# Optimization experiments

Measured on AMD Instinct MI355X. Metric: run time of the kernel, lower is better.

Reference implementation:

```python
import jax, jax.numpy as jnp
import numpy as np

W_WIN = 5        # fine_window_size
D_F = 128        # fine d_model
D_C = 256        # coarse d_model
B, HF, WF = 2, 208, 208
WC = 104
LC = WC * WC
N = 5000


def setup_inputs() -> dict:
    key = jax.random.key(0)
    ks = jax.random.split(key, 12)
    inp = {
        'feat_f0': jax.random.normal(ks[0], (B, D_F, HF, WF), jnp.float32),
        'feat_f1': jax.random.normal(ks[1], (B, D_F, HF, WF), jnp.float32),
        'feat_c0': jax.random.normal(ks[2], (B, LC, D_C), jnp.float32),
        'feat_c1': jax.random.normal(ks[3], (B, LC, D_C), jnp.float32),
        # linear layer params (stored as [in, out]; torch weight is [out, in])
        'corr_fuse_w': jax.random.normal(ks[4], (3 * D_F, D_F), jnp.float32) * 0.05,
        'corr_fuse_b': jnp.zeros((D_F,), jnp.float32),
        'down_proj_w': jax.random.normal(ks[5], (D_C, D_F), jnp.float32) * 0.05,
        'down_proj_b': jnp.zeros((D_F,), jnp.float32),
        'merge_feat_w': jax.random.normal(ks[6], (2 * D_F, D_F), jnp.float32) * 0.05,
        'merge_feat_b': jnp.zeros((D_F,), jnp.float32),
        'b_ids': jax.random.randint(ks[7], (N,), 0, B),
        'i_ids': jax.random.randint(ks[8], (N,), 0, LC),
        'j_ids': jax.random.randint(ks[9], (N,), 0, LC),
        'w0c': WC,
        'w1c': WC,
    }
    return inp


def _extract_patches(feat, b_ids, x_ids, y_ids, W):
    # Equivalent to F.unfold(feat, W, stride=1, padding=W//2) followed by a
    # gather at linear index y*width+x: directly gather the WxW window
    # centered at (x, y) with zero padding. feat: [B, C, H, Wd].
    Bsz, C, H, Wd = feat.shape
    off = jnp.arange(W) - W // 2
    yy = (y_ids[:, None] + off)[:, :, None]          # [n, W, 1]
    xx = (x_ids[:, None] + off)[:, None, :]          # [n, 1, W]
    valid = (yy >= 0) & (yy < H) & (xx >= 0) & (xx < Wd)  # [n, W, W]
    yc = jnp.clip(yy, 0, H - 1)
    xc = jnp.clip(xx, 0, Wd - 1)
    # advanced-index gather -> [n, W, W, C] (kernel rows outer, cols inner,
    # channel last: matches unfold's C-major layout after view/transpose)
    p = feat[b_ids[:, None, None], :, yc, xc]
    p = p * valid[..., None].astype(feat.dtype)
    return p.reshape(p.shape[0], W * W, C)           # [n, ww, C]


def reference(feat_f0, feat_f1, feat_c0, feat_c1,
              corr_fuse_w, corr_fuse_b, down_proj_w, down_proj_b,
              merge_feat_w, merge_feat_b,
              b_ids, i_ids, j_ids, w0c, w1c):
    W = W_WIN
    ww = W * W
    d_f = feat_f0.shape[1]
    Hf0, Wf0 = feat_f0.shape[2], feat_f0.shape[3]
    Hf1, Wf1 = feat_f1.shape[2], feat_f1.shape[3]

    x0 = jnp.clip((i_ids % w0c) * 2, 0, Wf0 - 1)
    y0 = jnp.clip((i_ids // w0c) * 2, 0, Hf0 - 1)
    x1 = jnp.clip((j_ids % w1c) * 2, 0, Wf1 - 1)
    y1 = jnp.clip((j_ids // w1c) * 2, 0, Hf1 - 1)

    p0 = _extract_patches(feat_f0, b_ids, x0, y0, W)   # [N, ww, d_f]
    p1 = _extract_patches(feat_f1, b_ids, x1, y1, W)

    inv_s = 1.0 / (d_f ** 0.5)
    c_patch = p0 * p1 * inv_s
    ctx_map = feat_f1.mean(axis=(2, 3))[b_ids][:, None, :]   # [N, 1, d_f]
    c_uav = p0 * ctx_map * inv_s
    ctx_uav = feat_f0.mean(axis=(2, 3))[b_ids][:, None, :]
    c_map = p1 * ctx_uav * inv_s

    f0 = jnp.concatenate([c_patch, c_uav, c_map], -1) @ corr_fuse_w + corr_fuse_b
    f1 = jnp.concatenate([c_patch, c_map, c_uav], -1) @ corr_fuse_w + corr_fuse_b

    # cat_c_feat branch
    fc = jnp.concatenate([feat_c0[b_ids, i_ids], feat_c1[b_ids, j_ids]], 0)
    fc = fc @ down_proj_w + down_proj_b                       # [2N, d_f]
    fc_rep = jnp.broadcast_to(fc[:, None, :], (fc.shape[0], ww, fc.shape[1]))
    merged = jnp.concatenate([jnp.concatenate([f0, f1], 0), fc_rep], -1)
    merged = merged @ merge_feat_w + merge_feat_b             # [2N, ww, d_f]

    n = f0.shape[0]
    return merged[:n], merged[n:]
```

## Files before the change

kernel.cpp:

```cpp
#include <hip/hip_runtime.h>

#define HF   208
#define WF   208
#define D_C  256
#define LC   10816
#define NPTS 5000
#define HW   (HF*WF)
#define INV_S 0.08838834764831845f
#define PAD  136

#define G_BLOCKS    625
#define PREP_BLOCKS 641
#define TR_BLOCKS   2704
#define PTG_GRID    (G_BLOCKS + PREP_BLOCKS + TR_BLOCKS)

typedef __bf16 bf16_t;
typedef __bf16 bf16x8 __attribute__((ext_vector_type(8)));
typedef float  f32x4  __attribute__((ext_vector_type(4)));

#define FTR_OFF   172032
#define FTR_BYTES ((size_t)2*2*HW*128*2)
#define G_OFF     (FTR_OFF + FTR_BYTES)
#define G_BYTES   ((size_t)2*NPTS*128*4)

__global__ __launch_bounds__(256, 8) void ptg_kernel(
    const float* __restrict__ f0, const float* __restrict__ f1,
    const float* __restrict__ fc0, const float* __restrict__ fc1,
    const float* __restrict__ corr_w, const float* __restrict__ corr_b,
    const float* __restrict__ dp_w,   const float* __restrict__ dp_b,
    const float* __restrict__ mg_w,   const float* __restrict__ mg_b,
    const int* __restrict__ b_ids, const int* __restrict__ i_ids,
    const int* __restrict__ j_ids,
    bf16_t* __restrict__ A_swz, bf16_t* __restrict__ DmB,
    float* __restrict__ bias_all,
    bf16_t* __restrict__ ftr, float* __restrict__ ctxs,
    float* __restrict__ g) {
  __shared__ __align__(16) union {
    struct { bf16_t tile[64][136]; float cred[128]; } tr;
    float s_src[16][256];
  } sm;
  int bid = blockIdx.x;
  int tid = threadIdx.x;

  int prep_id = -1;
  if (gridDim.x == 641) {
    prep_id = bid;
  } else if (bid >= G_BLOCKS && bid < G_BLOCKS + PREP_BLOCKS) {
    prep_id = bid - G_BLOCKS;
  }

  if (prep_id >= 0) {
    if (tid >= 128) return;
    int c = tid;
    if (prep_id < 384) {
      int mat = prep_id >> 7, r = prep_id & 127;
      float acc = 0.f;
      for (int t = 0; t < 128; ++t)
        acc += corr_w[(mat * 128 + r) * 128 + t] * mg_w[t * 128 + c];
      if (mat == 0) acc *= INV_S;
      int ks = r >> 5, quad = (r & 31) >> 3, jj = r & 7;
      int nt = c >> 4, lr = c & 15;
      A_swz[mat * 16384 + (((nt * 4 + ks) * 64) + quad * 16 + lr) * 8 + jj] = (bf16_t)acc;
    } else if (prep_id < 640) {
      int r = prep_id - 384;
      float acc = 0.f;
      for (int t = 0; t < 128; ++t)
        acc += dp_w[r * 128 + t] * mg_w[(128 + t) * 128 + c];
      DmB[(((r >> 3) * 128) + c) * 8 + (r & 7)] = (bf16_t)acc;
    } else {
      float acc = mg_b[c];
      for (int t = 0; t < 128; ++t) {
        acc += corr_b[t] * mg_w[t * 128 + c];
        acc += dp_b[t]   * mg_w[(128 + t) * 128 + c];
      }
      bias_all[c] = acc;
    }
    return;
  }

  if (bid < G_BLOCKS) {
    int r0 = bid * 16;
    for (int u = tid; u < 16 * 256; u += 256) {
      int rr = u >> 8, t = u & 255;
      int r = r0 + rr;
      const float* src;
      int b, idx;
      if (r < NPTS) { b = b_ids[r]; idx = i_ids[r]; src = fc0; }
      else          { b = b_ids[r - NPTS]; idx = j_ids[r - NPTS]; src = fc1; }
      sm.s_src[rr][t] = src[((size_t)b * LC + idx) * D_C + t];
    }
    __syncthreads();
    int col = tid & 127, half = tid >> 7;
    float h[8];
    {
      float db = dp_b[col];
#pragma unroll
      for (int r8 = 0; r8 < 8; ++r8) h[r8] = db;
      for (int t = 0; t < 256; t += 4) {
        f32x4 wv;
#pragma unroll
        for (int k = 0; k < 4; ++k) wv[k] = dp_w[(t + k) * 128 + col];
#pragma unroll
        for (int r8 = 0; r8 < 8; ++r8) {
          f32x4 sv = *(const f32x4*)&sm.s_src[half * 8 + r8][t];
          h[r8] += sv[0] * wv[0] + sv[1] * wv[1] + sv[2] * wv[2] + sv[3] * wv[3];
        }
      }
    }
    __syncthreads();
    float* s_h = &sm.s_src[0][0];
#pragma unroll
    for (int r8 = 0; r8 < 8; ++r8) s_h[(half * 8 + r8) * 128 + col] = h[r8];
    __syncthreads();
    float acc2[8];
    float mb = mg_b[col];
#pragma unroll
    for (int r8 = 0; r8 < 8; ++r8) acc2[r8] = mb;
    for (int t = 0; t < 128; t += 4) {
      f32x4 wv;
#pragma unroll
      for (int k = 0; k < 4; ++k) wv[k] = mg_w[(128 + t + k) * 128 + col];
#pragma unroll
      for (int r8 = 0; r8 < 8; ++r8) {
        f32x4 sv = *(const f32x4*)&s_h[(half * 8 + r8) * 128 + t];
        acc2[r8] += sv[0] * wv[0] + sv[1] * wv[1] + sv[2] * wv[2] + sv[3] * wv[3];
      }
    }
    float cp = 0.f;
    for (int t = 0; t < 128; ++t) cp += corr_b[t] * mg_w[t * 128 + col];
#pragma unroll
    for (int r8 = 0; r8 < 8; ++r8)
      g[(size_t)(r0 + half * 8 + r8) * 128 + col] = acc2[r8] + cp;
    return;
  }

  int tbid = bid - (G_BLOCKS + PREP_BLOCKS);
  int tb = tbid / 676;
  int hw0 = (tbid % 676) * 64;
  const float* src = (tb < 2 ? f0 : f1) + (size_t)((tb & 1) * 128) * HW;
  int wg = tid & 15, cr = tid >> 4;
  int w4 = wg * 4;
  float csum[8];
#pragma unroll
  for (int k = 0; k < 8; ++k) {
    int c = cr + k * 16;
    f32x4 v = *(const f32x4*)&src[(size_t)c * HW + hw0 + w4];
    csum[k] = (v[0] + v[1]) + (v[2] + v[3]);
#pragma unroll
    for (int j = 0; j < 4; ++j) sm.tr.tile[w4 + j][c] = (bf16_t)v[j];
  }
#pragma unroll
  for (int k = 0; k < 8; ++k) {
    float s = csum[k];
    s += __shfl_down(s, 8, 16);
    s += __shfl_down(s, 4, 16);
    s += __shfl_down(s, 2, 16);
    s += __shfl_down(s, 1, 16);
    if (wg == 0) sm.tr.cred[cr + k * 16] = s;
  }
  __syncthreads();
  if (tid < 128) atomicAdd(&ctxs[tb * 128 + tid], sm.tr.cred[tid]);
  bf16_t* dst = ftr + ((size_t)tb * HW + hw0) * 128;
  int cb = wg * 8;
#pragma unroll
  for (int i = 0; i < 4; ++i) {
    int p = cr + 16 * i;
    bf16x8 v = *(const bf16x8*)&sm.tr.tile[p][cb];
    *(bf16x8*)(dst + (size_t)p * 128 + cb) = v;
  }
}

__global__ __launch_bounds__(256, 6) void main_kernel(
    const bf16_t* __restrict__ ftr,
    const int* __restrict__ b_ids, const int* __restrict__ i_ids,
    const int* __restrict__ j_ids, const int* __restrict__ w0c_p,
    const int* __restrict__ w1c_p, const float* __restrict__ ctxs,
    const bf16_t* __restrict__ A_swz, const float* __restrict__ g,
    float* __restrict__ out) {
  __shared__ __align__(16) union {
    bf16_t sV[3][32][PAD];
    float  so[2][25 * 128];
  } sm;

  int n = blockIdx.x;
  int tid = threadIdx.x;
  int b = b_ids[n], ii = i_ids[n], jj = j_ids[n];
  int w0c = w0c_p[0], w1c = w1c_p[0];
  int x0 = min((ii % w0c) * 2, WF - 1), y0 = min((ii / w0c) * 2, HF - 1);
  int x1 = min((jj % w1c) * 2, WF - 1), y1 = min((jj / w1c) * 2, HF - 1);

  int grp = tid >> 3, e = tid & 7;
  if (grp < 25) {
    const bf16_t* base0 = ftr + (size_t)b * HW * 128;
    const bf16_t* base1 = ftr + (size_t)(2 + b) * HW * 128;
    int dy = grp / 5 - 2, dx = grp % 5 - 2;
    int ya = y0 + dy, xa = x0 + dx;
    int yb = y1 + dy, xb = x1 + dx;
    bool v0 = (ya >= 0 && ya < HF && xa >= 0 && xa < WF);
    bool v1 = (yb >= 0 && yb < HF && xb >= 0 && xb < WF);
    const bf16_t* r0 = base0 + ((size_t)(v0 ? ya * WF + xa : 0)) * 128;
    const bf16_t* r1 = base1 + ((size_t)(v1 ? yb * WF + xb : 0)) * 128;
    const float ksc = INV_S / (float)HW;
#pragma unroll
    for (int h = 0; h < 2; ++h) {
      int cb = h * 64 + e * 8;
      bf16x8 a0 = *(const bf16x8*)(r0 + cb);
      bf16x8 a1 = *(const bf16x8*)(r1 + cb);
      f32x4 cs0a = *(const f32x4*)&ctxs[b * 128 + cb];
      f32x4 cs0b = *(const f32x4*)&ctxs[b * 128 + cb + 4];
      f32x4 cs1a = *(const f32x4*)&ctxs[256 + b * 128 + cb];
      f32x4 cs1b = *(const f32x4*)&ctxs[256 + b * 128 + cb + 4];
      bf16x8 oP, o1, o2;
#pragma unroll
      for (int j = 0; j < 8; ++j) {
        float p0 = v0 ? (float)a0[j] : 0.f;
        float p1 = v1 ? (float)a1[j] : 0.f;
        float c0f = (j < 4 ? cs0a[j & 3] : cs0b[j & 3]) * ksc;
        float c1f = (j < 4 ? cs1a[j & 3] : cs1b[j & 3]) * ksc;
        oP[j] = (bf16_t)(p0 * p1);
        o1[j] = (bf16_t)(p0 * c1f);
        o2[j] = (bf16_t)(p1 * c0f);
      }
      *(bf16x8*)&sm.sV[0][grp][cb] = oP;
      *(bf16x8*)&sm.sV[1][grp][cb] = o1;
      *(bf16x8*)&sm.sV[2][grp][cb] = o2;
    }
  }
  __syncthreads();

  int w = tid >> 6, lane = tid & 63, quad = lane >> 4, lr = lane & 15;
  f32x4 accP[2][2] = {};
  f32x4 acc01[2][2] = {};
  f32x4 acc10[2][2] = {};

#pragma unroll
  for (int ks = 0; ks < 4; ++ks) {
    bf16x8 va[2][3];
#pragma unroll
    for (int mt = 0; mt < 2; ++mt)
#pragma unroll
      for (int m = 0; m < 3; ++m)
        va[mt][m] = *(const bf16x8*)&sm.sV[m][mt * 16 + lr][ks * 32 + quad * 8];
    bf16x8 vb[3][2];
#pragma unroll
    for (int m = 0; m < 3; ++m)
#pragma unroll
      for (int ntl = 0; ntl < 2; ++ntl) {
        int nt = w * 2 + ntl;
        vb[m][ntl] = *(const bf16x8*)(A_swz + m * 16384 + (((nt * 4 + ks) * 64) + lane) * 8);
      }
#pragma unroll
    for (int mt = 0; mt < 2; ++mt)
#pragma unroll
      for (int ntl = 0; ntl < 2; ++ntl) {
        accP[mt][ntl]  = __builtin_amdgcn_mfma_f32_16x16x32_bf16(va[mt][0], vb[0][ntl], accP[mt][ntl], 0, 0, 0);
        acc01[mt][ntl] = __builtin_amdgcn_mfma_f32_16x16x32_bf16(va[mt][1], vb[1][ntl], acc01[mt][ntl], 0, 0, 0);
        acc01[mt][ntl] = __builtin_amdgcn_mfma_f32_16x16x32_bf16(va[mt][2], vb[2][ntl], acc01[mt][ntl], 0, 0, 0);
        acc10[mt][ntl] = __builtin_amdgcn_mfma_f32_16x16x32_bf16(va[mt][2], vb[1][ntl], acc10[mt][ntl], 0, 0, 0);
        acc10[mt][ntl] = __builtin_amdgcn_mfma_f32_16x16x32_bf16(va[mt][1], vb[2][ntl], acc10[mt][ntl], 0, 0, 0);
      }
  }
  __syncthreads();

#pragma unroll
  for (int ntl = 0; ntl < 2; ++ntl) {
    int col = w * 32 + ntl * 16 + lr;
#pragma unroll
    for (int mt = 0; mt < 2; ++mt)
#pragma unroll
      for (int rg = 0; rg < 4; ++rg) {
        int row = mt * 16 + quad * 4 + rg;
        if (row < 25) {
          sm.so[0][row * 128 + col] = accP[mt][ntl][rg] + acc01[mt][ntl][rg];
          sm.so[1][row * 128 + col] = accP[mt][ntl][rg] + acc10[mt][ntl][rg];
        }
      }
  }
  __syncthreads();

  float* o0 = out + (size_t)n * 3200;
  float* o1 = out + (size_t)NPTS * 3200 + (size_t)n * 3200;
  const float* g0 = g + (size_t)n * 128;
  const float* g1 = g + (size_t)(NPTS + n) * 128;
  for (int i = tid; i < 800; i += 256) {
    int f = i * 4, c = f & 127;
    f32x4 gv0 = *(const f32x4*)(g0 + c);
    f32x4 gv1 = *(const f32x4*)(g1 + c);
    f32x4 v0 = *(const f32x4*)&sm.so[0][f];
    f32x4 v1 = *(const f32x4*)&sm.so[1][f];
    __builtin_nontemporal_store(v0 + gv0, (f32x4*)(o0 + f));
    __builtin_nontemporal_store(v1 + gv1, (f32x4*)(o1 + f));
  }
}

__global__ __launch_bounds__(256) void ctx_mean_f32_kernel(
    const float* __restrict__ f0, const float* __restrict__ f1,
    float* __restrict__ ctxs) {
  int id = blockIdx.x;
  const float* src = (id < 256 ? f0 : f1) + (size_t)(id & 255) * HW;
  float s = 0.f;
  for (int i = threadIdx.x; i < HW; i += 256) s += src[i];
  for (int off = 32; off > 0; off >>= 1) s += __shfl_down(s, off, 64);
  __shared__ float part[4];
  if ((threadIdx.x & 63) == 0) part[threadIdx.x >> 6] = s;
  __syncthreads();
  if (threadIdx.x == 0) ctxs[id] = part[0] + part[1] + part[2] + part[3];
}

__global__ __launch_bounds__(256, 4) void main_fallback_kernel(
    const float* __restrict__ f0, const float* __restrict__ f1,
    const float* __restrict__ fc0, const float* __restrict__ fc1,
    const int* __restrict__ b_ids, const int* __restrict__ i_ids,
    const int* __restrict__ j_ids, const int* __restrict__ w0c_p,
    const int* __restrict__ w1c_p, const float* __restrict__ ctxs,
    const float* __restrict__ bias_all, const bf16_t* __restrict__ A_swz,
    const bf16_t* __restrict__ DmB, float* __restrict__ out) {
  __shared__ __align__(16) bf16_t sV[3][32][PAD];
  __shared__ float sg[2][128];
  int n = blockIdx.x;
  int tid = threadIdx.x;
  int b = b_ids[n], ii = i_ids[n], jj = j_ids[n];
  int w0c = w0c_p[0], w1c = w1c_p[0];
  int x0 = min((ii % w0c) * 2, WF - 1), y0 = min((ii / w0c) * 2, HF - 1);
  int x1 = min((jj % w1c) * 2, WF - 1), y1 = min((jj / w1c) * 2, HF - 1);
  const float ksc = INV_S / (float)HW;
  int c = tid & 127, kh = tid >> 7;
  float cs0 = ctxs[b * 128 + c] * ksc;
  float cs1 = ctxs[256 + b * 128 + c] * ksc;
  const float* f0b = f0 + (size_t)(b * 128 + c) * HW;
  const float* f1b = f1 + (size_t)(b * 128 + c) * HW;
  for (int k = kh; k < 32; k += 2) {
    float p0 = 0.f, p1 = 0.f;
    if (k < 25) {
      int dy = k / 5 - 2, dx = k % 5 - 2;
      int ya = y0 + dy, xa = x0 + dx;
      if (ya >= 0 && ya < HF && xa >= 0 && xa < WF) p0 = f0b[ya * WF + xa];
      int yb = y1 + dy, xb = x1 + dx;
      if (yb >= 0 && yb < HF && xb >= 0 && xb < WF) p1 = f1b[yb * WF + xb];
    }
    sV[0][k][c] = (bf16_t)(p0 * p1);
    sV[1][k][c] = (bf16_t)(p0 * cs1);
    sV[2][k][c] = (bf16_t)(p1 * cs0);
  }
  {
    int h = tid >> 7, col = tid & 127;
    const float* fcrow = h ? fc1 + ((size_t)b * LC + jj) * D_C
                           : fc0 + ((size_t)b * LC + ii) * D_C;
    const bf16_t* dbase = DmB + col * 8;
    float p0 = 0.f, p1 = 0.f, p2 = 0.f, p3 = 0.f;
#pragma unroll 4
    for (int t8 = 0; t8 < 32; ++t8) {
      bf16x8 d  = *(const bf16x8*)(dbase + t8 * 1024);
      f32x4  fa = *(const f32x4*)(fcrow + t8 * 8);
      f32x4  fb = *(const f32x4*)(fcrow + t8 * 8 + 4);
      p0 += fa[0] * (float)d[0] + fb[0] * (float)d[4];
      p1 += fa[1] * (float)d[1] + fb[1] * (float)d[5];
      p2 += fa[2] * (float)d[2] + fb[2] * (float)d[6];
      p3 += fa[3] * (float)d[3] + fb[3] * (float)d[7];
    }
    sg[h][col] = ((p0 + p1) + (p2 + p3));
  }
  __syncthreads();
  int w = tid >> 6, lane = tid & 63, quad = lane >> 4, lr = lane & 15;
  f32x4 accP[2][2] = {}, acc01[2][2] = {}, acc10[2][2] = {};
#pragma unroll
  for (int ks = 0; ks < 4; ++ks) {
    bf16x8 va[2][3];
#pragma unroll
    for (int mt = 0; mt < 2; ++mt)
#pragma unroll
      for (int m = 0; m < 3; ++m)
        va[mt][m] = *(const bf16x8*)&sV[m][mt * 16 + lr][ks * 32 + quad * 8];
    bf16x8 vb[3][2];
#pragma unroll
    for (int m = 0; m < 3; ++m)
#pragma unroll
      for (int ntl = 0; ntl < 2; ++ntl) {
        int nt = w * 2 + ntl;
        vb[m][ntl] = *(const bf16x8*)(A_swz + m * 16384 + (((nt * 4 + ks) * 64) + lane) * 8);
      }
#pragma unroll
    for (int mt = 0; mt < 2; ++mt)
#pragma unroll
      for (int ntl = 0; ntl < 2; ++ntl) {
        accP[mt][ntl]  = __builtin_amdgcn_mfma_f32_16x16x32_bf16(va[mt][0], vb[0][ntl], accP[mt][ntl], 0, 0, 0);
        acc01[mt][ntl] = __builtin_amdgcn_mfma_f32_16x16x32_bf16(va[mt][1], vb[1][ntl], acc01[mt][ntl], 0, 0, 0);
        acc01[mt][ntl] = __builtin_amdgcn_mfma_f32_16x16x32_bf16(va[mt][2], vb[2][ntl], acc01[mt][ntl], 0, 0, 0);
        acc10[mt][ntl] = __builtin_amdgcn_mfma_f32_16x16x32_bf16(va[mt][2], vb[1][ntl], acc10[mt][ntl], 0, 0, 0);
        acc10[mt][ntl] = __builtin_amdgcn_mfma_f32_16x16x32_bf16(va[mt][1], vb[2][ntl], acc10[mt][ntl], 0, 0, 0);
      }
  }
#pragma unroll
  for (int ntl = 0; ntl < 2; ++ntl) {
    int col = w * 32 + ntl * 16 + lr;
    float bg = bias_all[col];
    float gg0 = sg[0][col] + bg, gg1 = sg[1][col] + bg;
#pragma unroll
    for (int mt = 0; mt < 2; ++mt)
#pragma unroll
      for (int rg = 0; rg < 4; ++rg) {
        int row = mt * 16 + quad * 4 + rg;
        if (row < 25) {
          size_t o = ((size_t)n * 25 + row) * 128 + col;
          out[o] = accP[mt][ntl][rg] + acc01[mt][ntl][rg] + gg0;
          out[(size_t)NPTS * 25 * 128 + o] = accP[mt][ntl][rg] + acc10[mt][ntl][rg] + gg1;
        }
      }
  }
}

extern "C" void kernel_launch(void* const* d_in, const int* in_sizes, int n_in,
                              void* d_out, int out_size, void* d_ws, size_t ws_size,
                              hipStream_t stream) {
  const float* f0     = (const float*)d_in[0];
  const float* f1     = (const float*)d_in[1];
  const float* fc0    = (const float*)d_in[2];
  const float* fc1    = (const float*)d_in[3];
  const float* corr_w = (const float*)d_in[4];
  const float* corr_b = (const float*)d_in[5];
  const float* dp_w   = (const float*)d_in[6];
  const float* dp_b   = (const float*)d_in[7];
  const float* mg_w   = (const float*)d_in[8];
  const float* mg_b   = (const float*)d_in[9];
  const int* b_ids    = (const int*)d_in[10];
  const int* i_ids    = (const int*)d_in[11];
  const int* j_ids    = (const int*)d_in[12];
  const int* w0c      = (const int*)d_in[13];
  const int* w1c      = (const int*)d_in[14];

  char* ws = (char*)d_ws;
  float*  ctxs     = (float*)(ws);
  float*  bias_all = (float*)(ws + 4096);
  bf16_t* A_swz    = (bf16_t*)(ws + 8192);
  bf16_t* DmB      = (bf16_t*)(ws + 106496);
  bf16_t* ftr      = (bf16_t*)(ws + FTR_OFF);
  float*  g        = (float*)(ws + G_OFF);
  int fast = (ws_size >= G_OFF + G_BYTES) ? 1 : 0;

  if (fast) {
    hipMemsetAsync(ctxs, 0, 2048, stream);
    ptg_kernel<<<PTG_GRID, 256, 0, stream>>>(
        f0, f1, fc0, fc1, corr_w, corr_b, dp_w, dp_b, mg_w, mg_b,
        b_ids, i_ids, j_ids, A_swz, DmB, bias_all, ftr, ctxs, g);
    main_kernel<<<NPTS, 256, 0, stream>>>(ftr, b_ids, i_ids, j_ids, w0c, w1c,
                                          ctxs, A_swz, g, (float*)d_out);
  } else {
    ptg_kernel<<<641, 256, 0, stream>>>(
        f0, f1, fc0, fc1, corr_w, corr_b, dp_w, dp_b, mg_w, mg_b,
        b_ids, i_ids, j_ids, A_swz, DmB, bias_all, ftr, ctxs, g);
    ctx_mean_f32_kernel<<<512, 256, 0, stream>>>(f0, f1, ctxs);
    main_fallback_kernel<<<NPTS, 256, 0, stream>>>(f0, f1, fc0, fc1, b_ids,
                                                   i_ids, j_ids, w0c, w1c, ctxs,
                                                   bias_all, A_swz, DmB,
                                                   (float*)d_out);
  }
}
```

Measured before the change: 330.0 us.

## Vectorize coarse-feature GEMV blocks and swizzle transpose tile to avoid bank conflicts

The G blocks in the prep kernel now use f32x4 loads for the gathered coarse rows and weights. Each thread computes 4 output columns for 2 rows, and the redundant per-thread corr_b·mg_w dot product is dropped. That bias term now comes from bias_all, which main_kernel adds in its epilogue. The transpose blocks load all 8 vectors first, then write into LDS with an XOR swizzle on the channel index, cutting LDS bank conflicts during the bf16 transpose. This adds one extra bias load per output vector in main_kernel.

Result: faster. 322.6 us (-2.3%).

```diff
diff --git a/kernel.cpp b/kernel.cpp
--- a/kernel.cpp
+++ b/kernel.cpp
@@ -80,57 +80,52 @@
 
   if (bid < G_BLOCKS) {
     int r0 = bid * 16;
-    for (int u = tid; u < 16 * 256; u += 256) {
-      int rr = u >> 8, t = u & 255;
-      int r = r0 + rr;
-      const float* src;
-      int b, idx;
-      if (r < NPTS) { b = b_ids[r]; idx = i_ids[r]; src = fc0; }
-      else          { b = b_ids[r - NPTS]; idx = j_ids[r - NPTS]; src = fc1; }
-      sm.s_src[rr][t] = src[((size_t)b * LC + idx) * D_C + t];
+    {
+      int l = tid & 63, wv = tid >> 6;
+      for (int k2 = 0; k2 < 4; ++k2) {
+        int rr = wv * 4 + k2;
+        int r = r0 + rr;
+        const float* src;
+        int b, idx;
+        if (r < NPTS) { b = b_ids[r]; idx = i_ids[r]; src = fc0; }
+        else          { b = b_ids[r - NPTS]; idx = j_ids[r - NPTS]; src = fc1; }
+        f32x4 val = *(const f32x4*)&src[((size_t)b * LC + idx) * D_C + l * 4];
+        *(f32x4*)&sm.s_src[rr][l * 4] = val;
+      }
     }
     __syncthreads();
-    int col = tid & 127, half = tid >> 7;
-    float h[8];
-    {
-      float db = dp_b[col];
-#pragma unroll
-      for (int r8 = 0; r8 < 8; ++r8) h[r8] = db;
-      for (int t = 0; t < 256; t += 4) {
-        f32x4 wv;
-#pragma unroll
-        for (int k = 0; k < 4; ++k) wv[k] = dp_w[(t + k) * 128 + col];
-#pragma unroll
-        for (int r8 = 0; r8 < 8; ++r8) {
-          f32x4 sv = *(const f32x4*)&sm.s_src[half * 8 + r8][t];
-          h[r8] += sv[0] * wv[0] + sv[1] * wv[1] + sv[2] * wv[2] + sv[3] * wv[3];
-        }
-      }
+    int cg = tid & 31, rg = tid >> 5;
+    const f32x4* dpw4 = (const f32x4*)dp_w;
+    f32x4 h0 = {0.f, 0.f, 0.f, 0.f}, h1 = {0.f, 0.f, 0.f, 0.f};
+    for (int t = 0; t < 256; t += 4) {
+      f32x4 w0 = dpw4[(t + 0) * 32 + cg];
+      f32x4 w1 = dpw4[(t + 1) * 32 + cg];
+      f32x4 w2 = dpw4[(t + 2) * 32 + cg];
+      f32x4 w3 = dpw4[(t + 3) * 32 + cg];
+      f32x4 s0 = *(const f32x4*)&sm.s_src[rg * 2][t];
+      f32x4 s1 = *(const f32x4*)&sm.s_src[rg * 2 + 1][t];
+      h0 += w0 * s0[0] + w1 * s0[1] + w2 * s0[2] + w3 * s0[3];
+      h1 += w0 * s1[0] + w1 * s1[1] + w2 * s1[2] + w3 * s1[3];
     }
     __syncthreads();
     float* s_h = &sm.s_src[0][0];
-#pragma unroll
-    for (int r8 = 0; r8 < 8; ++r8) s_h[(half * 8 + r8) * 128 + col] = h[r8];
+    *(f32x4*)&s_h[(rg * 2) * 128 + cg * 4]     = h0;
+    *(f32x4*)&s_h[(rg * 2 + 1) * 128 + cg * 4] = h1;
     __syncthreads();
-    float acc2[8];
-    float mb = mg_b[col];
-#pragma unroll
-    for (int r8 = 0; r8 < 8; ++r8) acc2[r8] = mb;
+    const f32x4* mgw4 = (const f32x4*)(mg_w + 128 * 128);
+    f32x4 a0 = {0.f, 0.f, 0.f, 0.f}, a1 = {0.f, 0.f, 0.f, 0.f};
     for (int t = 0; t < 128; t += 4) {
-      f32x4 wv;
-#pragma unroll
-      for (int k = 0; k < 4; ++k) wv[k] = mg_w[(128 + t + k) * 128 + col];
-#pragma unroll
-      for (int r8 = 0; r8 < 8; ++r8) {
-        f32x4 sv = *(const f32x4*)&s_h[(half * 8 + r8) * 128 + t];
-        acc2[r8] += sv[0] * wv[0] + sv[1] * wv[1] + sv[2] * wv[2] + sv[3] * wv[3];
-      }
-    }
-    float cp = 0.f;
-    for (int t = 0; t < 128; ++t) cp += corr_b[t] * mg_w[t * 128 + col];
-#pragma unroll
-    for (int r8 = 0; r8 < 8; ++r8)
-      g[(size_t)(r0 + half * 8 + r8) * 128 + col] = acc2[r8] + cp;
+      f32x4 w0 = mgw4[(t + 0) * 32 + cg];
+      f32x4 w1 = mgw4[(t + 1) * 32 + cg];
+      f32x4 w2 = mgw4[(t + 2) * 32 + cg];
+      f32x4 w3 = mgw4[(t + 3) * 32 + cg];
+      f32x4 s0 = *(const f32x4*)&s_h[(rg * 2) * 128 + t];
+      f32x4 s1 = *(const f32x4*)&s_h[(rg * 2 + 1) * 128 + t];
+      a0 += w0 * s0[0] + w1 * s0[1] + w2 * s0[2] + w3 * s0[3];
+      a1 += w0 * s1[0] + w1 * s1[1] + w2 * s1[2] + w3 * s1[3];
+    }
+    *(f32x4*)&g[(size_t)(r0 + rg * 2) * 128 + cg * 4]     = a0;
+    *(f32x4*)&g[(size_t)(r0 + rg * 2 + 1) * 128 + cg * 4] = a1;
     return;
   }
 
@@ -140,14 +135,21 @@
   const float* src = (tb < 2 ? f0 : f1) + (size_t)((tb & 1) * 128) * HW;
   int wg = tid & 15, cr = tid >> 4;
   int w4 = wg * 4;
-  float csum[8];
+  f32x4 v[8];
 #pragma unroll
   for (int k = 0; k < 8; ++k) {
     int c = cr + k * 16;
-    f32x4 v = *(const f32x4*)&src[(size_t)c * HW + hw0 + w4];
-    csum[k] = (v[0] + v[1]) + (v[2] + v[3]);
-#pragma unroll
-    for (int j = 0; j < 4; ++j) sm.tr.tile[w4 + j][c] = (bf16_t)v[j];
+    v[k] = *(const f32x4*)&src[(size_t)c * HW + hw0 + w4];
+  }
+  float csum[8];
+  int wmask = wg & 7;
+#pragma unroll
+  for (int k = 0; k < 8; ++k) {
+    int c = cr + k * 16;
+    csum[k] = (v[k][0] + v[k][1]) + (v[k][2] + v[k][3]);
+    int cs = (((c >> 3) ^ wmask) << 3) | (c & 7);
+#pragma unroll
+    for (int j = 0; j < 4; ++j) sm.tr.tile[w4 + j][cs] = (bf16_t)v[k][j];
   }
 #pragma unroll
   for (int k = 0; k < 8; ++k) {
@@ -161,12 +163,12 @@
   __syncthreads();
   if (tid < 128) atomicAdd(&ctxs[tb * 128 + tid], sm.tr.cred[tid]);
   bf16_t* dst = ftr + ((size_t)tb * HW + hw0) * 128;
-  int cb = wg * 8;
 #pragma unroll
   for (int i = 0; i < 4; ++i) {
     int p = cr + 16 * i;
-    bf16x8 v = *(const bf16x8*)&sm.tr.tile[p][cb];
-    *(bf16x8*)(dst + (size_t)p * 128 + cb) = v;
+    int cs = (wg ^ ((p >> 2) & 7)) << 3;
+    bf16x8 vv = *(const bf16x8*)&sm.tr.tile[p][cs];
+    *(bf16x8*)(dst + (size_t)p * 128 + wg * 8) = vv;
   }
 }
 
@@ -176,7 +178,7 @@
     const int* __restrict__ j_ids, const int* __restrict__ w0c_p,
     const int* __restrict__ w1c_p, const float* __restrict__ ctxs,
     const bf16_t* __restrict__ A_swz, const float* __restrict__ g,
-    float* __restrict__ out) {
+    const float* __restrict__ bias_all, float* __restrict__ out) {
   __shared__ __align__(16) union {
     bf16_t sV[3][32][PAD];
     float  so[2][25 * 128];
@@ -284,8 +286,9 @@
   const float* g1 = g + (size_t)(NPTS + n) * 128;
   for (int i = tid; i < 800; i += 256) {
     int f = i * 4, c = f & 127;
-    f32x4 gv0 = *(const f32x4*)(g0 + c);
-    f32x4 gv1 = *(const f32x4*)(g1 + c);
+    f32x4 bv  = *(const f32x4*)(bias_all + c);
+    f32x4 gv0 = *(const f32x4*)(g0 + c) + bv;
+    f32x4 gv1 = *(const f32x4*)(g1 + c) + bv;
     f32x4 v0 = *(const f32x4*)&sm.so[0][f];
     f32x4 v1 = *(const f32x4*)&sm.so[1][f];
     __builtin_nontemporal_store(v0 + gv0, (f32x4*)(o0 + f));
@@ -443,7 +446,8 @@
         f0, f1, fc0, fc1, corr_w, corr_b, dp_w, dp_b, mg_w, mg_b,
         b_ids, i_ids, j_ids, A_swz, DmB, bias_all, ftr, ctxs, g);
     main_kernel<<<NPTS, 256, 0, stream>>>(ftr, b_ids, i_ids, j_ids, w0c, w1c,
-                                          ctxs, A_swz, g, (float*)d_out);
+                                          ctxs, A_swz, g, bias_all,
+                                          (float*)d_out);
   } else {
     ptg_kernel<<<641, 256, 0, stream>>>(
         f0, f1, fc0, fc1, corr_w, corr_b, dp_w, dp_b, mg_w, mg_b,
```
